# Optimization experiments

Measured on AMD Instinct MI355X. Metric: run time of the kernel, lower is better.

The kernel has to match this reference:

```python
import jax, jax.numpy as jnp
import numpy as np

KH, KW, STRIDE, PAD = 3, 3, 1, 1
TREE_DEPTH = 3
NUM_LEAVES = 2 ** TREE_DEPTH  # 8
NUM_NODES = NUM_LEAVES - 1    # 7
OUT_CH, IN_CH = 256, 64
B, H, W = 16, 48, 48
PATCH_LEN = IN_CH * KH * KW   # 576

# Each of the 16 relaxed binary logic gates g_k(a,b) is affine in (1, a, b, a*b):
#   g_k(a,b) = c0 + c1*a + c2*b + c3*(a*b)
# Rows follow the standard difflogic gate ordering (gate 3 = pass-through a).
GATE_COEFF = np.array([
    [0.,  0.,  0.,  0.],   # 0: FALSE
    [0.,  0.,  0.,  1.],   # 1: a AND b
    [0.,  1.,  0., -1.],   # 2: a AND NOT b
    [0.,  1.,  0.,  0.],   # 3: a
    [0.,  0.,  1., -1.],   # 4: NOT a AND b
    [0.,  0.,  1.,  0.],   # 5: b
    [0.,  1.,  1., -2.],   # 6: a XOR b
    [0.,  1.,  1., -1.],   # 7: a OR b
    [1., -1., -1.,  1.],   # 8: NOT (a OR b)
    [1., -1., -1.,  2.],   # 9: NOT (a XOR b)
    [1.,  0., -1.,  0.],   # 10: NOT b
    [1.,  0., -1.,  1.],   # 11: a OR NOT b
    [1., -1.,  0.,  0.],   # 12: NOT a
    [1., -1.,  0.,  1.],   # 13: NOT a OR b
    [1.,  0.,  0., -1.],   # 14: NOT (a AND b)
    [1.,  0.,  0.,  0.],   # 15: TRUE
], dtype=np.float32)


def _unfold(x):
    # x: (B, C, Hp, Wp) -> (B, C*KH*KW, Ho*Wo), channel-major then row-major
    # kernel ordering (matches torch.nn.functional.unfold).
    b, c, hp, wp = x.shape
    ho = (hp - KH) // STRIDE + 1
    wo = (wp - KW) // STRIDE + 1
    cols = jnp.stack(
        [x[:, :, i:i + STRIDE * ho:STRIDE, j:j + STRIDE * wo:STRIDE]
         for i in range(KH) for j in range(KW)], axis=2)  # (B, C, KH*KW, Ho, Wo)
    return cols.reshape(b, c * KH * KW, ho * wo), ho, wo


def setup_inputs() -> dict:
    key = jax.random.key(0)
    k1, k2, k3 = jax.random.split(key, 3)
    x = jax.random.uniform(k1, (B, IN_CH, H, W), dtype=jnp.float32)
    logits = jax.random.normal(k2, (OUT_CH, NUM_NODES, 16), dtype=jnp.float32)
    leaf_indices = jax.random.randint(k3, (OUT_CH, NUM_LEAVES), 0, PATCH_LEN, dtype=jnp.int32)
    return {"x": x, "logits": logits, "leaf_indices": leaf_indices}


def reference(x, logits, leaf_indices):
    b = x.shape[0]
    o = logits.shape[0]
    xp = jnp.pad(x, ((0, 0), (0, 0), (PAD, PAD), (PAD, PAD)))
    patches, ho, wo = _unfold(xp)          # (B, patch_len, L)
    cur = patches[:, leaf_indices, :]      # gather leaves: (B, O, num_leaves, L)
    coeff = jnp.asarray(GATE_COEFF)        # (16, 4)
    node_ptr = 0
    width = NUM_LEAVES
    for _ in range(TREE_DEPTH):
        nc = width // 2
        a = cur[:, :, 0::2, :]             # (B, O, nc, L)
        bb = cur[:, :, 1::2, :]
        probs = jax.nn.softmax(logits[:, node_ptr:node_ptr + nc, :], axis=-1)  # (O, nc, 16)
        # softmax-weighted mixture of the 16 gates = affine combo in (1, a, b, ab)
        w = jnp.einsum('ong,gc->onc', probs, coeff)  # (O, nc, 4)
        w = w[None, :, :, :, None]                   # (1, O, nc, 4, 1)
        cur = w[:, :, :, 0] + w[:, :, :, 1] * a + w[:, :, :, 2] * bb + w[:, :, :, 3] * (a * bb)
        node_ptr += nc
        width = nc
    y = cur[:, :, 0, :]                    # (B, O, L)
    return y.reshape(b, o, ho, wo)
```

## Files before the change

### kernel.cpp

```cpp
#include <hip/hip_runtime.h>

#define NB 16
#define IN_CH 64
#define OUT_CH 256
#define NH 48
#define NW 48
#define NPIX (NH * NW)
#define ROW_STRIDE 52
#define CH_STRIDE (4 * ROW_STRIDE)
#define LDS_DW (IN_CH * CH_STRIDE)
#define NITEMS (IN_CH * 4 * 26)
#define META_F4 9

__constant__ float c_gate[16 * 4] = {
    0.f, 0.f, 0.f, 0.f,
    0.f, 0.f, 0.f, 1.f,
    0.f, 1.f, 0.f, -1.f,
    0.f, 1.f, 0.f, 0.f,
    0.f, 0.f, 1.f, -1.f,
    0.f, 0.f, 1.f, 0.f,
    0.f, 1.f, 1.f, -2.f,
    0.f, 1.f, 1.f, -1.f,
    1.f, -1.f, -1.f, 1.f,
    1.f, -1.f, -1.f, 2.f,
    1.f, 0.f, -1.f, 0.f,
    1.f, 0.f, -1.f, 1.f,
    1.f, -1.f, 0.f, 0.f,
    1.f, -1.f, 0.f, 1.f,
    1.f, 0.f, 0.f, -1.f,
    1.f, 0.f, 0.f, 0.f
};

__global__ __launch_bounds__(256) void prep_kernel(
    const float* __restrict__ logits,
    const int*   __restrict__ leaf_idx,
    float*       __restrict__ meta)
{
    int t = blockIdx.x * 256 + threadIdx.x;
    if (t < OUT_CH * 8) {
        int idx = leaf_idx[t];
        int c  = idx / 9;
        int k  = idx - c * 9;
        int di = k / 3;
        int dj = k - di * 3;
        reinterpret_cast<int*>(meta)[(t >> 3) * 36 + (t & 7)] =
            c * CH_STRIDE + di * ROW_STRIDE + dj;
    } else {
        int t2 = t - OUT_CH * 8;
        if (t2 >= OUT_CH * 7) return;
        int o = t2 / 7;
        int n = t2 - o * 7;
        const float* lg = logits + (size_t)t2 * 16;

        float m = lg[0];
#pragma unroll
        for (int g = 1; g < 16; ++g) m = fmaxf(m, lg[g]);
        float e16[16];
        float s = 0.f;
#pragma unroll
        for (int g = 0; g < 16; ++g) { e16[g] = expf(lg[g] - m); s += e16[g]; }
        float inv = 1.f / s;

        float w0 = 0.f, w1 = 0.f, w2 = 0.f, w3 = 0.f;
#pragma unroll
        for (int g = 0; g < 16; ++g) {
            float p = e16[g] * inv;
            w0 += p * c_gate[g * 4 + 0];
            w1 += p * c_gate[g * 4 + 1];
            w2 += p * c_gate[g * 4 + 2];
            w3 += p * c_gate[g * 4 + 3];
        }
        float* mw = meta + o * 36 + 8 + n * 4;
        mw[0] = w0; mw[1] = w1; mw[2] = w2; mw[3] = w3;
    }
}

__global__ __launch_bounds__(512, 6) void ltc_kernel(
    const float*  __restrict__ x,
    const float4* __restrict__ meta,
    float*        __restrict__ out)
{
    __shared__ float lds[LDS_DW];

    const int band  = blockIdx.x;
    const int ohalf = blockIdx.y;
    const int b     = blockIdx.z;
    const int r0    = band * 2;
    const int tid   = threadIdx.x;

    const float* xb = x + (size_t)b * IN_CH * NPIX;
    for (int it = tid; it < NITEMS; it += 512) {
        int c   = it / 104;
        int rem = it - c * 104;
        int r4  = rem / 26;
        int p   = rem - r4 * 26;
        int gr  = r0 - 1 + r4;
        float2 v = make_float2(0.f, 0.f);
        if (p > 0 && p < 25 && (unsigned)gr < NH)
            v = *reinterpret_cast<const float2*>(xb + (c * NH + gr) * NW + (2 * p - 2));
        *reinterpret_cast<float2*>(&lds[c * CH_STRIDE + r4 * ROW_STRIDE + 2 * p]) = v;
    }
    __syncthreads();

    const int lane = tid & 63;
    const int wid  = tid >> 6;
    const int og   = lane >> 5;
    const int pxg  = lane & 31;
    const int o0   = ohalf * 128 + ((wid << 1) | og) * 8;

    int bases[3], opx[3];
#pragma unroll
    for (int g = 0; g < 3; ++g) {
        int px = g * 32 + pxg;
        int rr = (px >= 48) ? 1 : 0;
        int cc = px - rr * 48;
        bases[g] = rr * ROW_STRIDE + cc + 1;
        opx[g]   = (r0 + rr) * NW + cc;
    }

    const float4* mptr  = meta + (size_t)o0 * META_F4;
    float*        pbase = out + ((size_t)b * OUT_CH + o0) * NPIX;

#pragma unroll 2
    for (int i = 0; i < 8; ++i) {
        float4 M[9];
#pragma unroll
        for (int q = 0; q < 9; ++q) M[q] = mptr[q];

        const int off0 = __float_as_int(M[0].x);
        const int off1 = __float_as_int(M[0].y);
        const int off2 = __float_as_int(M[0].z);
        const int off3 = __float_as_int(M[0].w);
        const int off4 = __float_as_int(M[1].x);
        const int off5 = __float_as_int(M[1].y);
        const int off6 = __float_as_int(M[1].z);
        const int off7 = __float_as_int(M[1].w);

#pragma unroll
        for (int g = 0; g < 3; ++g) {
            const int bg = bases[g];
            float v0 = lds[off0 + bg];
            float v1 = lds[off1 + bg];
            float v2 = lds[off2 + bg];
            float v3 = lds[off3 + bg];
            float v4 = lds[off4 + bg];
            float v5 = lds[off5 + bg];
            float v6 = lds[off6 + bg];
            float v7 = lds[off7 + bg];
            float t0 = fmaf(v1, fmaf(M[2].w, v0, M[2].z), fmaf(M[2].y, v0, M[2].x));
            float t1 = fmaf(v3, fmaf(M[3].w, v2, M[3].z), fmaf(M[3].y, v2, M[3].x));
            float t2 = fmaf(v5, fmaf(M[4].w, v4, M[4].z), fmaf(M[4].y, v4, M[4].x));
            float t3 = fmaf(v7, fmaf(M[5].w, v6, M[5].z), fmaf(M[5].y, v6, M[5].x));
            float u0 = fmaf(t1, fmaf(M[6].w, t0, M[6].z), fmaf(M[6].y, t0, M[6].x));
            float u1 = fmaf(t3, fmaf(M[7].w, t2, M[7].z), fmaf(M[7].y, t2, M[7].x));
            float y  = fmaf(u1, fmaf(M[8].w, u0, M[8].z), fmaf(M[8].y, u0, M[8].x));
            pbase[opx[g]] = y;
        }
        mptr  += META_F4;
        pbase += NPIX;
    }
}

extern "C" void kernel_launch(void* const* d_in, const int* in_sizes, int n_in,
                              void* d_out, int out_size, void* d_ws, size_t ws_size,
                              hipStream_t stream) {
    const float* x        = (const float*)d_in[0];
    const float* logits   = (const float*)d_in[1];
    const int*   leaf_idx = (const int*)d_in[2];
    float*       out      = (float*)d_out;
    float*       meta     = (float*)d_ws;

    prep_kernel<<<15, 256, 0, stream>>>(logits, leaf_idx, meta);

    dim3 grid(24, 2, NB);
    ltc_kernel<<<grid, 512, 0, stream>>>(x, (const float4*)meta, out);
}
```

Before: 33.49 us.

## Remap lanes to 16 pixels x 4 output channels, six pixels per thread

Changes the thread-to-work mapping in the main kernel. Each wave now covers 4 output-channel groups of 16 pixels instead of 2 groups of 32, and each thread evaluates 6 pixels over 4 output channels instead of 3 pixels over 8. Each channel's metadata load is therefore shared across more pixels, and the per-pixel base/row index arithmetic becomes fixed immediate offsets. The loop is no longer unrolled, which trades instruction-level overlap between channels for lower register pressure. Stores become 16-wide segments rather than 32-wide, which may reduce write coalescing.

```diff
diff --git a/kernel.cpp b/kernel.cpp
--- a/kernel.cpp
+++ b/kernel.cpp
@@ -75,6 +75,20 @@
     }
 }
 
+__device__ __forceinline__ float tree_eval(
+    const float* v,
+    const float4& W0, const float4& W1, const float4& W2, const float4& W3,
+    const float4& W4, const float4& W5, const float4& W6)
+{
+    float t0 = fmaf(v[1], fmaf(W0.w, v[0], W0.z), fmaf(W0.y, v[0], W0.x));
+    float t1 = fmaf(v[3], fmaf(W1.w, v[2], W1.z), fmaf(W1.y, v[2], W1.x));
+    float t2 = fmaf(v[5], fmaf(W2.w, v[4], W2.z), fmaf(W2.y, v[4], W2.x));
+    float t3 = fmaf(v[7], fmaf(W3.w, v[6], W3.z), fmaf(W3.y, v[6], W3.x));
+    float u0 = fmaf(t1, fmaf(W4.w, t0, W4.z), fmaf(W4.y, t0, W4.x));
+    float u1 = fmaf(t3, fmaf(W5.w, t2, W5.z), fmaf(W5.y, t2, W5.x));
+    return fmaf(u1, fmaf(W6.w, u0, W6.z), fmaf(W6.y, u0, W6.x));
+}
+
 __global__ __launch_bounds__(512, 6) void ltc_kernel(
     const float*  __restrict__ x,
     const float4* __restrict__ meta,
@@ -104,58 +118,51 @@
 
     const int lane = tid & 63;
     const int wid  = tid >> 6;
-    const int og   = lane >> 5;
-    const int pxg  = lane & 31;
-    const int o0   = ohalf * 128 + ((wid << 1) | og) * 8;
-
-    int bases[3], opx[3];
-#pragma unroll
-    for (int g = 0; g < 3; ++g) {
-        int px = g * 32 + pxg;
-        int rr = (px >= 48) ? 1 : 0;
-        int cc = px - rr * 48;
-        bases[g] = rr * ROW_STRIDE + cc + 1;
-        opx[g]   = (r0 + rr) * NW + cc;
-    }
+    const int q    = lane >> 4;
+    const int pxg  = lane & 15;
+    const int o0   = ohalf * 128 + ((wid << 2) | q) * 4;
+    const int cbase = pxg + 1;
 
     const float4* mptr  = meta + (size_t)o0 * META_F4;
-    float*        pbase = out + ((size_t)b * OUT_CH + o0) * NPIX;
+    float*        pbase = out + ((size_t)b * OUT_CH + o0) * NPIX + r0 * NW + pxg;
 
-#pragma unroll 2
-    for (int i = 0; i < 8; ++i) {
-        float4 M[9];
-#pragma unroll
-        for (int q = 0; q < 9; ++q) M[q] = mptr[q];
+#pragma unroll 1
+    for (int i = 0; i < 4; ++i) {
+        float4 M0 = mptr[0], M1 = mptr[1];
+        float4 W0 = mptr[2], W1 = mptr[3], W2 = mptr[4];
+        float4 W3 = mptr[5], W4 = mptr[6], W5 = mptr[7], W6 = mptr[8];
 
-        const int off0 = __float_as_int(M[0].x);
-        const int off1 = __float_as_int(M[0].y);
-        const int off2 = __float_as_int(M[0].z);
-        const int off3 = __float_as_int(M[0].w);
-        const int off4 = __float_as_int(M[1].x);
-        const int off5 = __float_as_int(M[1].y);
-        const int off6 = __float_as_int(M[1].z);
-        const int off7 = __float_as_int(M[1].w);
+        int vb[8];
+        vb[0] = __float_as_int(M0.x) + cbase;
+        vb[1] = __float_as_int(M0.y) + cbase;
+        vb[2] = __float_as_int(M0.z) + cbase;
+        vb[3] = __float_as_int(M0.w) + cbase;
+        vb[4] = __float_as_int(M1.x) + cbase;
+        vb[5] = __float_as_int(M1.y) + cbase;
+        vb[6] = __float_as_int(M1.z) + cbase;
+        vb[7] = __float_as_int(M1.w) + cbase;
+
+        float va[8], vc[8];
+        float y0, y1;
 
 #pragma unroll
-        for (int g = 0; g < 3; ++g) {
-            const int bg = bases[g];
-            float v0 = lds[off0 + bg];
-            float v1 = lds[off1 + bg];
-            float v2 = lds[off2 + bg];
-            float v3 = lds[off3 + bg];
-            float v4 = lds[off4 + bg];
-            float v5 = lds[off5 + bg];
-            float v6 = lds[off6 + bg];
-            float v7 = lds[off7 + bg];
-            float t0 = fmaf(v1, fmaf(M[2].w, v0, M[2].z), fmaf(M[2].y, v0, M[2].x));
-            float t1 = fmaf(v3, fmaf(M[3].w, v2, M[3].z), fmaf(M[3].y, v2, M[3].x));
-            float t2 = fmaf(v5, fmaf(M[4].w, v4, M[4].z), fmaf(M[4].y, v4, M[4].x));
-            float t3 = fmaf(v7, fmaf(M[5].w, v6, M[5].z), fmaf(M[5].y, v6, M[5].x));
-            float u0 = fmaf(t1, fmaf(M[6].w, t0, M[6].z), fmaf(M[6].y, t0, M[6].x));
-            float u1 = fmaf(t3, fmaf(M[7].w, t2, M[7].z), fmaf(M[7].y, t2, M[7].x));
-            float y  = fmaf(u1, fmaf(M[8].w, u0, M[8].z), fmaf(M[8].y, u0, M[8].x));
-            pbase[opx[g]] = y;
-        }
+        for (int j = 0; j < 8; ++j) { va[j] = lds[vb[j]]; vc[j] = lds[vb[j] + 16]; }
+        y0 = tree_eval(va, W0, W1, W2, W3, W4, W5, W6);
+        y1 = tree_eval(vc, W0, W1, W2, W3, W4, W5, W6);
+        pbase[0]  = y0; pbase[16] = y1;
+
+#pragma unroll
+        for (int j = 0; j < 8; ++j) { va[j] = lds[vb[j] + 52]; vc[j] = lds[vb[j] + 68]; }
+        y0 = tree_eval(va, W0, W1, W2, W3, W4, W5, W6);
+        y1 = tree_eval(vc, W0, W1, W2, W3, W4, W5, W6);
+        pbase[48] = y0; pbase[64] = y1;
+
+#pragma unroll
+        for (int j = 0; j < 8; ++j) { va[j] = lds[vb[j] + 32]; vc[j] = lds[vb[j] + 84]; }
+        y0 = tree_eval(va, W0, W1, W2, W3, W4, W5, W6);
+        y1 = tree_eval(vc, W0, W1, W2, W3, W4, W5, W6);
+        pbase[32] = y0; pbase[80] = y1;
+
         mptr  += META_F4;
         pbase += NPIX;
     }
```

Measured after the change: 95.02 us. +183.8%, slower.
